# Kernel tuning notes

Measured on AMD Instinct MI355X. Metric: run time of the kernel, lower is better.

## Reference

```python
import jax, jax.numpy as jnp
import numpy as np

N_NODES = 20000
N_EDGES = 160000
N_GRAPHS = 64
EMB_DIM = 16
N_BASIS = 16
MAX_RADIUS = 5.0
MUL_IN = 8   # output_size: multiplicity of scalar atom features
MUL_OUT = 4  # multiplicity per output irrep (4x0e + 4x1o + 4x2e -> dim 36)
W_NUMEL = 3 * MUL_IN * MUL_IN * MUL_OUT  # 768 per-edge tensor-product weights


def setup_inputs() -> dict:
    key = jax.random.key(0)
    ks = jax.random.split(key, 16)
    pos = jax.random.normal(ks[0], (N_NODES, 3), jnp.float32) * 3.0
    A = jax.random.randint(ks[1], (N_NODES,), 0, 10)
    batch = jnp.sort(jax.random.randint(ks[2], (N_NODES,), 0, N_GRAPHS))
    edge_src = jax.random.randint(ks[3], (N_EDGES,), 0, N_NODES)
    edge_dst = jax.random.randint(ks[4], (N_EDGES,), 0, N_NODES)
    edge_shifts = jnp.zeros((N_EDGES, 3), jnp.float32)
    cell = jnp.broadcast_to(jnp.eye(3, dtype=jnp.float32) * 10.0, (N_GRAPHS, 3, 3))
    emb_table = jax.random.normal(ks[5], (10, EMB_DIM), jnp.float32)
    fit_w1 = jax.random.normal(ks[6], (EMB_DIM, 64), jnp.float32) * (2.0 / EMB_DIM) ** 0.5
    fit_b1 = jnp.zeros((64,), jnp.float32)
    fit_w2 = jax.random.normal(ks[7], (64, 32), jnp.float32) * (2.0 / 64.0) ** 0.5
    fit_b2 = jnp.zeros((32,), jnp.float32)
    fit_w3 = jax.random.normal(ks[8], (32, MUL_IN), jnp.float32) * (2.0 / 32.0) ** 0.5
    fit_b3 = jnp.zeros((MUL_IN,), jnp.float32)
    fc_w1 = jax.random.normal(ks[9], (N_BASIS, 64), jnp.float32)
    fc_w2 = jax.random.normal(ks[10], (64, 64), jnp.float32)
    fc_w3 = jax.random.normal(ks[11], (64, 64), jnp.float32)
    fc_w4 = jax.random.normal(ks[12], (64, W_NUMEL), jnp.float32)
    return dict(pos=pos, A=A, batch=batch, edge_src=edge_src, edge_dst=edge_dst,
                edge_shifts=edge_shifts, cell=cell, emb_table=emb_table,
                fit_w1=fit_w1, fit_b1=fit_b1, fit_w2=fit_w2, fit_b2=fit_b2,
                fit_w3=fit_w3, fit_b3=fit_b3,
                fc_w1=fc_w1, fc_w2=fc_w2, fc_w3=fc_w3, fc_w4=fc_w4)


def _forward(pos, edge_shifts, cell, emb_table, fit_w1, fit_b1, fit_w2, fit_b2,
             fit_w3, fit_b3, fc_w1, fc_w2, fc_w3, fc_w4, A, batch, edge_src, edge_dst):
    E = edge_src.shape[0]
    # edge vectors with periodic shifts
    shift = jnp.einsum('ni,nij->nj', edge_shifts, cell[batch[edge_src]])
    ev = pos[edge_dst] - pos[edge_src] + shift                     # [E,3]
    r = jnp.sqrt(jnp.sum(ev * ev, axis=1))                         # [E]
    v = ev / jnp.maximum(r, 1e-9)[:, None]
    x, y, z = v[:, 0], v[:, 1], v[:, 2]
    # spherical harmonics lmax=2, normalize=True, 'component' normalization (e3nn order)
    sh0 = jnp.ones_like(x)                                         # [E]
    sh1 = jnp.sqrt(3.0) * jnp.stack([y, z, x], axis=-1)            # [E,3]
    s15 = jnp.sqrt(15.0); s5 = jnp.sqrt(5.0)
    sh2 = jnp.stack([s15 * x * y, s15 * y * z, (s5 / 2.0) * (3.0 * z * z - 1.0),
                     s15 * x * z, (s15 / 2.0) * (x * x - y * y)], axis=-1)  # [E,5]
    # node scalar features: embedding + fitnet MLP (SiLU)
    h = jax.nn.silu(emb_table[A] @ fit_w1 + fit_b1)
    h = jax.nn.silu(h @ fit_w2 + fit_b2)
    Ai = h @ fit_w3 + fit_b3                                       # [N, MUL_IN]
    # soft_one_hot_linspace(gaussian, cutoff=True) * sqrt(n_basis)
    centers = jnp.linspace(0.0, MAX_RADIUS, N_BASIS + 2)[1:-1]
    step = centers[1] - centers[0]
    rb = jnp.exp(-(((r[:, None] - centers) / step) ** 2)) / 1.12 * jnp.sqrt(jnp.float32(N_BASIS))
    # radial net -> per-edge tensor-product weights (e3nn FullyConnectedNet style, no bias)
    g = jax.nn.silu(rb @ fc_w1 / jnp.sqrt(jnp.float32(N_BASIS)))
    g = jax.nn.silu(g @ fc_w2 / 8.0)
    g = jax.nn.silu(g @ fc_w3 / 8.0)
    w = (g @ fc_w4 / 8.0).reshape(E, 3, MUL_IN, MUL_IN, MUL_OUT)   # [E,3 paths,u,v,w]
    # FullTensorProduct(Ai_src, sh) then FullyConnectedTensorProduct(., Ai_dst) with
    # per-edge weights; scalar x irrep paths factorize: out_l[e,w,m] = S_l[e,w]*sh_l[e,m]
    P = Ai[edge_src][:, :, None] * Ai[edge_dst][:, None, :]        # [E,u,v]
    S = jnp.einsum('euv,eluvw->elw', P, w) / jnp.float32(MUL_IN)   # path norm 1/sqrt(u*v)
    out0 = S[:, 0, :] * sh0[:, None]                               # [E,4]
    out1 = (S[:, 1, :, None] * sh1[:, None, :]).reshape(E, MUL_OUT * 3)
    out2 = (S[:, 2, :, None] * sh2[:, None, :]).reshape(E, MUL_OUT * 5)
    ef = jnp.concatenate([out0, out1, out2], axis=-1)              # [E,36]
    # scatter-mean to destination nodes
    cnt = jnp.clip(jax.ops.segment_sum(jnp.ones((E,), ef.dtype), edge_dst,
                                       num_segments=N_NODES), 1.0)
    return jax.ops.segment_sum(ef, edge_dst, num_segments=N_NODES) / cnt[:, None]


def reference(pos, A, batch, edge_src, edge_dst, edge_shifts, cell, emb_table,
              fit_w1, fit_b1, fit_w2, fit_b2, fit_w3, fit_b3,
              fc_w1, fc_w2, fc_w3, fc_w4):
    return _forward(pos, edge_shifts, cell, emb_table, fit_w1, fit_b1, fit_w2,
                    fit_b2, fit_w3, fit_b3, fc_w1, fc_w2, fc_w3, fc_w4,
                    A, batch, edge_src, edge_dst)
```

## Files before the change

kernel.cpp:

```cpp
#include <hip/hip_runtime.h>
#include <math.h>

#define N_NODES 20000
#define N_EDGES 160000

#define NBINS   512
#define BINS1   513
#define RMAX    7.5f

static const size_t OFF_EF  = 0;
static const size_t OFF_T   = OFF_EF  + (size_t)N_EDGES * 16 * 4;
static const size_t OFF_G   = OFF_T   + (size_t)100 * 64 * 12 * 4;
static const size_t OFF_SV  = OFF_G   + (size_t)64 * BINS1 * 4;
static const size_t OFF_NOFF= OFF_SV  + (size_t)100 * BINS1 * 12 * 4;
static const size_t OFF_NCNT= OFF_NOFF+ (size_t)(N_NODES + 1) * 4;
static const size_t OFF_NCUR= OFF_NCNT+ (size_t)N_NODES * 4;

#define P1_T_BLOCKS  25
#define P1_G_BLOCKS  9
#define P1_H_BLOCKS  625
#define P1_GRID (P1_T_BLOCKS + P1_G_BLOCKS + P1_H_BLOCKS)
#define P2_SCAN_BLOCKS 79
#define P2_CHUNKS 9
#define P2_GRID (P2_SCAN_BLOCKS + 100 * P2_CHUNKS)

__device__ __forceinline__ float silu_f(float x) {
    return x / (1.0f + __expf(-x));
}

__global__ __launch_bounds__(256) void prep1_kernel(
        const float* __restrict__ emb,
        const float* __restrict__ fw1, const float* __restrict__ fb1,
        const float* __restrict__ fw2, const float* __restrict__ fb2,
        const float* __restrict__ fw3, const float* __restrict__ fb3,
        const float* __restrict__ fc_w1, const float* __restrict__ fc_w2,
        const float* __restrict__ fc_w3, const float* __restrict__ fc_w4,
        const int* __restrict__ edst,
        float* __restrict__ T, float* __restrict__ g_tT,
        int* __restrict__ cnt_i) {
    __shared__ float smem[4096];
    int b = blockIdx.x;
    int tid = threadIdx.x;

    if (b < P1_T_BLOCKS) {
        float* h1s = smem;
        float* h2s = smem + 640;
        float* ai  = smem + 960;
        for (int idx = tid; idx < 640; idx += 256) {
            int t = idx >> 6, j = idx & 63;
            float acc = fb1[j];
            #pragma unroll
            for (int i = 0; i < 16; i++) acc += emb[t * 16 + i] * fw1[i * 64 + j];
            h1s[idx] = silu_f(acc);
        }
        __syncthreads();
        for (int idx = tid; idx < 320; idx += 256) {
            int t = idx >> 5, j = idx & 31;
            float acc = fb2[j];
            #pragma unroll
            for (int i = 0; i < 64; i++) acc += h1s[t * 64 + i] * fw2[i * 32 + j];
            h2s[idx] = silu_f(acc);
        }
        __syncthreads();
        if (tid < 80) {
            int t = tid >> 3, j = tid & 7;
            float acc = fb3[j];
            #pragma unroll
            for (int i = 0; i < 32; i++) acc += h2s[t * 32 + i] * fw3[i * 8 + j];
            ai[tid] = acc;
        }
        __syncthreads();

        int idx = b * 256 + tid;
        int pair = idx >> 6;
        int k = idx & 63;
        int ts = pair / 10, td = pair - ts * 10;
        float a[8], bb[8];
        #pragma unroll
        for (int i = 0; i < 8; i++) a[i] = ai[ts * 8 + i];
        #pragma unroll
        for (int i = 0; i < 8; i++) bb[i] = ai[td * 8 + i];
        float sv[12];
        #pragma unroll
        for (int i = 0; i < 12; i++) sv[i] = 0.0f;
        const float* wk = fc_w4 + k * 768;
        #pragma unroll 2
        for (int u = 0; u < 8; u++) {
            #pragma unroll
            for (int v = 0; v < 8; v++) {
                float ab = a[u] * bb[v];
                const float* wp = wk + u * 32 + v * 4;
                float4 w0 = *(const float4*)(wp);
                float4 w1 = *(const float4*)(wp + 256);
                float4 w2 = *(const float4*)(wp + 512);
                sv[0] += ab * w0.x; sv[1] += ab * w0.y; sv[2]  += ab * w0.z; sv[3]  += ab * w0.w;
                sv[4] += ab * w1.x; sv[5] += ab * w1.y; sv[6]  += ab * w1.z; sv[7]  += ab * w1.w;
                sv[8] += ab * w2.x; sv[9] += ab * w2.y; sv[10] += ab * w2.z; sv[11] += ab * w2.w;
            }
        }
        float* tp = T + pair * 768 + k * 12;
        #pragma unroll
        for (int j = 0; j < 12; j++) tp[j] = sv[j];
    } else if (b < P1_T_BLOCKS + P1_G_BLOCKS) {
        int lane = tid & 63;
        int wq = __builtin_amdgcn_readfirstlane(tid >> 6);
        int bin = (b - P1_T_BLOCKS) * 64 + lane;
        bool valid = (bin <= NBINS);
        float r = (float)bin * (RMAX / (float)NBINS);

        float rb[16];
        const float step = 5.0f / 17.0f;
        const float istep = 17.0f / 5.0f;
        const float rsc = 4.0f / 1.12f;
        #pragma unroll
        for (int i = 0; i < 16; i++) {
            float dd = (r - (float)(i + 1) * step) * istep;
            rb[i] = __expf(-dd * dd) * rsc;
        }

        #pragma unroll
        for (int jj = 0; jj < 16; jj++) {
            int j = wq * 16 + jj;
            float a0 = 0, a1 = 0, a2 = 0, a3 = 0;
            #pragma unroll
            for (int i = 0; i < 16; i += 4) {
                a0 += rb[i]     * fc_w1[(i)     * 64 + j];
                a1 += rb[i + 1] * fc_w1[(i + 1) * 64 + j];
                a2 += rb[i + 2] * fc_w1[(i + 2) * 64 + j];
                a3 += rb[i + 3] * fc_w1[(i + 3) * 64 + j];
            }
            smem[j * 64 + lane] = silu_f(((a0 + a1) + (a2 + a3)) * 0.25f);
        }
        __syncthreads();

        float acc[16];
        #pragma unroll
        for (int jj = 0; jj < 16; jj++) acc[jj] = 0.0f;
        #pragma unroll
        for (int c = 0; c < 4; c++) {
            float hc[16];
            #pragma unroll
            for (int i = 0; i < 16; i++) hc[i] = smem[(c * 16 + i) * 64 + lane];
            #pragma unroll
            for (int jj = 0; jj < 16; jj++) {
                int j = wq * 16 + jj;
                #pragma unroll
                for (int i = 0; i < 16; i++) acc[jj] += hc[i] * fc_w2[(c * 16 + i) * 64 + j];
            }
        }
        __syncthreads();
        #pragma unroll
        for (int jj = 0; jj < 16; jj++) smem[(wq * 16 + jj) * 64 + lane] = silu_f(acc[jj] * 0.125f);
        __syncthreads();

        #pragma unroll
        for (int jj = 0; jj < 16; jj++) acc[jj] = 0.0f;
        #pragma unroll
        for (int c = 0; c < 4; c++) {
            float hc[16];
            #pragma unroll
            for (int i = 0; i < 16; i++) hc[i] = smem[(c * 16 + i) * 64 + lane];
            #pragma unroll
            for (int jj = 0; jj < 16; jj++) {
                int j = wq * 16 + jj;
                #pragma unroll
                for (int i = 0; i < 16; i++) acc[jj] += hc[i] * fc_w3[(c * 16 + i) * 64 + j];
            }
        }
        if (valid) {
            #pragma unroll
            for (int jj = 0; jj < 16; jj++)
                g_tT[(size_t)(wq * 16 + jj) * BINS1 + bin] = silu_f(acc[jj] * 0.125f);
        }
    } else {
        int e = (b - P1_T_BLOCKS - P1_G_BLOCKS) * 256 + tid;
        if (e < N_EDGES) atomicAdd(&cnt_i[edst[e]], 1);
    }
}

__global__ __launch_bounds__(256) void prep2_kernel(
        const int* __restrict__ cnt_i, int* __restrict__ node_off,
        const float* __restrict__ T, const float* __restrict__ g_tT,
        float* __restrict__ sv_table) {
    __shared__ float smem[4096];
    int b = blockIdx.x;
    int tid = threadIdx.x;

    if (b < P2_SCAN_BLOCKS) {
        int* wred = (int*)smem;
        int* wsum = (int*)smem + 4;
        int lane = tid & 63, w = tid >> 6;
        int nbase = b * 256;
        int n = nbase + tid;
        int c = (n < N_NODES) ? cnt_i[n] : 0;

        int part = 0;
        for (int i = tid; i < nbase; i += 256) part += cnt_i[i];
        #pragma unroll
        for (int off = 1; off < 64; off <<= 1) part += __shfl_xor(part, off);
        if (lane == 0) wred[w] = part;

        int sc = c;
        #pragma unroll
        for (int off = 1; off < 64; off <<= 1) {
            int v2 = __shfl_up(sc, off);
            if (lane >= off) sc += v2;
        }
        if (lane == 63) wsum[w] = sc;
        __syncthreads();

        int base = wred[0] + wred[1] + wred[2] + wred[3];
        int wb = 0;
        #pragma unroll
        for (int i = 0; i < 4; i++) wb += (i < w) ? wsum[i] : 0;
        if (n < N_NODES) node_off[n] = base + wb + (sc - c);
        if (b == 0 && tid == 0) node_off[N_NODES] = N_EDGES;
        return;
    }

    int idx = b - P2_SCAN_BLOCKS;
    int pair = idx / P2_CHUNKS;
    int chunk = idx - pair * P2_CHUNKS;

    float* part = smem;
    float* Tlds = smem + 3328;

    const float* Tp = T + pair * 768;
    #pragma unroll
    for (int i = tid; i < 768; i += 256) Tlds[i] = Tp[i];
    __syncthreads();

    int lane = tid & 63;
    int wq = tid >> 6;
    int bin = chunk * 64 + lane;
    bool valid = (bin <= NBINS);
    int rb = valid ? bin : NBINS;

    float acc[12];
    #pragma unroll
    for (int j = 0; j < 12; j++) acc[j] = 0.0f;
    #pragma unroll
    for (int kk = 0; kk < 16; kk++) {
        int k = wq * 16 + kk;
        float g = g_tT[(size_t)k * BINS1 + rb];
        const float* Tl = Tlds + k * 12;
        #pragma unroll
        for (int j = 0; j < 12; j++) acc[j] += g * Tl[j];
    }

    float* pp = part + (size_t)wq * 64 * 13 + (size_t)lane * 13;
    #pragma unroll
    for (int j = 0; j < 12; j++) pp[j] = acc[j];
    __syncthreads();

    const float isc = 1.0f / 64.0f;
    float* svp = sv_table + (size_t)pair * BINS1 * 12 + (size_t)chunk * 64 * 12;
    #pragma unroll
    for (int i = 0; i < 3; i++) {
        int o = tid + 256 * i;
        int bl = o / 12;
        int j = o - bl * 12;
        if (chunk * 64 + bl <= NBINS) {
            float s = part[(size_t)0 * 832 + bl * 13 + j]
                    + part[(size_t)1 * 832 + bl * 13 + j]
                    + part[(size_t)2 * 832 + bl * 13 + j]
                    + part[(size_t)3 * 832 + bl * 13 + j];
            svp[o] = s * isc;
        }
    }
}

__global__ __launch_bounds__(256) void edge_table_kernel(
        const float* __restrict__ pos, const int* __restrict__ batch,
        const int* __restrict__ esrc, const int* __restrict__ edst,
        const float* __restrict__ shifts, const float* __restrict__ cell,
        const int* __restrict__ A,
        const int* __restrict__ node_off, int* __restrict__ node_cur,
        const float* __restrict__ sv_table, float* __restrict__ ef) {
    int e = blockIdx.x * 256 + threadIdx.x;
    if (e >= N_EDGES) return;

    int s = esrc[e], d = edst[e];
    int slot = atomicAdd(&node_cur[d], 1);
    int base = node_off[d];

    int gb = batch[s];
    float t0 = shifts[e * 3 + 0], t1 = shifts[e * 3 + 1], t2 = shifts[e * 3 + 2];
    const float* C = cell + gb * 9;
    float shx = t0 * C[0] + t1 * C[3] + t2 * C[6];
    float shy = t0 * C[1] + t1 * C[4] + t2 * C[7];
    float shz = t0 * C[2] + t1 * C[5] + t2 * C[8];
    float ex = pos[d * 3 + 0] - pos[s * 3 + 0] + shx;
    float ey = pos[d * 3 + 1] - pos[s * 3 + 1] + shy;
    float ez = pos[d * 3 + 2] - pos[s * 3 + 2] + shz;
    float r = sqrtf(ex * ex + ey * ey + ez * ez);
    float inv = 1.0f / fmaxf(r, 1e-9f);
    float x = ex * inv, y = ey * inv, z = ez * inv;

    float sv[12];
    if (r >= RMAX) {
        #pragma unroll
        for (int j = 0; j < 12; j++) sv[j] = 0.0f;
    } else {
        int pair = A[s] * 10 + A[d];
        float t = r * ((float)NBINS / RMAX);
        int i = (int)t;
        i = (i > NBINS - 1) ? (NBINS - 1) : i;
        float f = t - (float)i;
        const float* r0 = sv_table + ((size_t)pair * BINS1 + i) * 12;
        #pragma unroll
        for (int j = 0; j < 12; j++) {
            float lo = r0[j], hi = r0[12 + j];
            sv[j] = lo + f * (hi - lo);
        }
    }

    float4* dst = (float4*)(ef + (size_t)(base + slot) * 16);
    dst[0] = make_float4(sv[0], sv[1], sv[2],  sv[3]);
    dst[1] = make_float4(sv[4], sv[5], sv[6],  sv[7]);
    dst[2] = make_float4(sv[8], sv[9], sv[10], sv[11]);
    dst[3] = make_float4(x, y, z, 0.0f);
}

__global__ __launch_bounds__(256) void gather_kernel(const float* __restrict__ ef,
                                                     const int* __restrict__ node_off,
                                                     float* __restrict__ out) {
    int t = blockIdx.x * 256 + threadIdx.x;
    if (t >= N_NODES * 8) return;
    int n = t >> 3;
    int q = t & 7;
    int beg = node_off[n], end = node_off[n + 1];
    const float4* ef4 = (const float4*)ef;

    const float S3  = 1.7320508075688772f;
    const float S15 = 3.8729833462074170f;
    const float S5  = 2.2360679774997896f;

    float acc[36];
    #pragma unroll
    for (int j = 0; j < 36; j++) acc[j] = 0.0f;

    for (int p = beg + q; p < end; p += 8) {
        const float4* rp = ef4 + (size_t)p * 4;
        float4 svA = rp[0];
        float4 svB = rp[1];
        float4 svC = rp[2];
        float4 dv  = rp[3];
        float x = dv.x, y = dv.y, z = dv.z;
        float sh1v[3] = { S3 * y, S3 * z, S3 * x };
        float sh2v[5] = { S15 * x * y, S15 * y * z, 0.5f * S5 * (3.0f * z * z - 1.0f),
                          S15 * x * z, 0.5f * S15 * (x * x - y * y) };
        acc[0] += svA.x; acc[1] += svA.y; acc[2] += svA.z; acc[3] += svA.w;
        float bw[4] = { svB.x, svB.y, svB.z, svB.w };
        #pragma unroll
        for (int w = 0; w < 4; w++) {
            #pragma unroll
            for (int j = 0; j < 3; j++) acc[4 + w * 3 + j] += bw[w] * sh1v[j];
        }
        float cw[4] = { svC.x, svC.y, svC.z, svC.w };
        #pragma unroll
        for (int w = 0; w < 4; w++) {
            #pragma unroll
            for (int j = 0; j < 5; j++) acc[16 + w * 5 + j] += cw[w] * sh2v[j];
        }
    }

    #pragma unroll
    for (int j = 0; j < 36; j++) {
        acc[j] += __shfl_xor(acc[j], 1);
        acc[j] += __shfl_xor(acc[j], 2);
        acc[j] += __shfl_xor(acc[j], 4);
    }

    if (q == 0) {
        float c = 1.0f / fmaxf((float)(end - beg), 1.0f);
        float4* o4 = (float4*)out + (size_t)n * 9;
        #pragma unroll
        for (int k = 0; k < 9; k++)
            o4[k] = make_float4(acc[k * 4 + 0] * c, acc[k * 4 + 1] * c,
                                acc[k * 4 + 2] * c, acc[k * 4 + 3] * c);
    }
}

extern "C" void kernel_launch(void* const* d_in, const int* in_sizes, int n_in,
                              void* d_out, int out_size, void* d_ws, size_t ws_size,
                              hipStream_t stream) {
    const float* pos    = (const float*)d_in[0];
    const int*   A      = (const int*)d_in[1];
    const int*   batch  = (const int*)d_in[2];
    const int*   esrc   = (const int*)d_in[3];
    const int*   edst   = (const int*)d_in[4];
    const float* shifts = (const float*)d_in[5];
    const float* cell   = (const float*)d_in[6];
    const float* emb    = (const float*)d_in[7];
    const float* fw1    = (const float*)d_in[8];
    const float* fb1    = (const float*)d_in[9];
    const float* fw2    = (const float*)d_in[10];
    const float* fb2    = (const float*)d_in[11];
    const float* fw3    = (const float*)d_in[12];
    const float* fb3    = (const float*)d_in[13];
    const float* fcw1   = (const float*)d_in[14];
    const float* fcw2   = (const float*)d_in[15];
    const float* fcw3   = (const float*)d_in[16];
    const float* fcw4   = (const float*)d_in[17];
    float* out = (float*)d_out;

    char* ws = (char*)d_ws;
    float* ef      = (float*)(ws + OFF_EF);
    float* T       = (float*)(ws + OFF_T);
    float* g_tT    = (float*)(ws + OFF_G);
    float* sv_table= (float*)(ws + OFF_SV);
    int*   node_off= (int*)(ws + OFF_NOFF);
    int*   cnt_i   = (int*)(ws + OFF_NCNT);
    int*   node_cur= (int*)(ws + OFF_NCUR);

    hipMemsetAsync(cnt_i, 0, (size_t)2 * N_NODES * 4, stream);

    prep1_kernel<<<P1_GRID, 256, 0, stream>>>(emb, fw1, fb1, fw2, fb2, fw3, fb3,
                                              fcw1, fcw2, fcw3, fcw4, edst,
                                              T, g_tT, cnt_i);
    prep2_kernel<<<P2_GRID, 256, 0, stream>>>(cnt_i, node_off, T, g_tT, sv_table);
    edge_table_kernel<<<(N_EDGES + 255) / 256, 256, 0, stream>>>(
        pos, batch, esrc, edst, shifts, cell, A, node_off, node_cur, sv_table, ef);
    gather_kernel<<<(N_NODES * 8 + 255) / 256, 256, 0, stream>>>(ef, node_off, out);
}
```

Baseline: 163.7 us.

## Fuse four pipeline kernels into one cooperative persistent kernel with grid syncs

Merges the prep1, prep2, edge-table and gather kernels into a single cooperative kernel of 640 persistent blocks. Each block loops over the old virtual block indices and the phases are separated by grid.sync() instead of kernel boundaries. This targets launch overhead and inter-kernel gaps. In exchange it adds grid-wide barrier cost, reduces parallelism in phases that previously had more blocks, and adds extra __syncthreads for shared-memory reuse. The old four-launch path remains as a fallback if the cooperative launch fails.

```diff
diff --git a/kernel.cpp b/kernel.cpp
--- a/kernel.cpp
+++ b/kernel.cpp
@@ -1,5 +1,8 @@
 #include <hip/hip_runtime.h>
+#include <hip/hip_cooperative_groups.h>
 #include <math.h>
+
+namespace cg = cooperative_groups;
 
 #define N_NODES 20000
 #define N_EDGES 160000
@@ -24,11 +27,14 @@
 #define P2_CHUNKS 9
 #define P2_GRID (P2_SCAN_BLOCKS + 100 * P2_CHUNKS)
 
+#define FGRID 640
+
 __device__ __forceinline__ float silu_f(float x) {
     return x / (1.0f + __expf(-x));
 }
 
-__global__ __launch_bounds__(256) void prep1_kernel(
+
+__device__ __forceinline__ void phaseA_body(int bb, int tid, float* smem,
         const float* __restrict__ emb,
         const float* __restrict__ fw1, const float* __restrict__ fb1,
         const float* __restrict__ fw2, const float* __restrict__ fb2,
@@ -38,11 +44,7 @@
         const int* __restrict__ edst,
         float* __restrict__ T, float* __restrict__ g_tT,
         int* __restrict__ cnt_i) {
-    __shared__ float smem[4096];
-    int b = blockIdx.x;
-    int tid = threadIdx.x;
-
-    if (b < P1_T_BLOCKS) {
+    if (bb < P1_T_BLOCKS) {
         float* h1s = smem;
         float* h2s = smem + 640;
         float* ai  = smem + 960;
@@ -71,15 +73,15 @@
         }
         __syncthreads();
 
-        int idx = b * 256 + tid;
+        int idx = bb * 256 + tid;
         int pair = idx >> 6;
         int k = idx & 63;
         int ts = pair / 10, td = pair - ts * 10;
-        float a[8], bb[8];
+        float a[8], bbv[8];
         #pragma unroll
         for (int i = 0; i < 8; i++) a[i] = ai[ts * 8 + i];
         #pragma unroll
-        for (int i = 0; i < 8; i++) bb[i] = ai[td * 8 + i];
+        for (int i = 0; i < 8; i++) bbv[i] = ai[td * 8 + i];
         float sv[12];
         #pragma unroll
         for (int i = 0; i < 12; i++) sv[i] = 0.0f;
@@ -88,7 +90,7 @@
         for (int u = 0; u < 8; u++) {
             #pragma unroll
             for (int v = 0; v < 8; v++) {
-                float ab = a[u] * bb[v];
+                float ab = a[u] * bbv[v];
                 const float* wp = wk + u * 32 + v * 4;
                 float4 w0 = *(const float4*)(wp);
                 float4 w1 = *(const float4*)(wp + 256);
@@ -101,10 +103,11 @@
         float* tp = T + pair * 768 + k * 12;
         #pragma unroll
         for (int j = 0; j < 12; j++) tp[j] = sv[j];
-    } else if (b < P1_T_BLOCKS + P1_G_BLOCKS) {
+        __syncthreads();
+    } else if (bb < P1_T_BLOCKS + P1_G_BLOCKS) {
         int lane = tid & 63;
         int wq = __builtin_amdgcn_readfirstlane(tid >> 6);
-        int bin = (b - P1_T_BLOCKS) * 64 + lane;
+        int bin = (bb - P1_T_BLOCKS) * 64 + lane;
         bool valid = (bin <= NBINS);
         float r = (float)bin * (RMAX / (float)NBINS);
 
@@ -172,25 +175,22 @@
             for (int jj = 0; jj < 16; jj++)
                 g_tT[(size_t)(wq * 16 + jj) * BINS1 + bin] = silu_f(acc[jj] * 0.125f);
         }
+        __syncthreads();
     } else {
-        int e = (b - P1_T_BLOCKS - P1_G_BLOCKS) * 256 + tid;
+        int e = (bb - P1_T_BLOCKS - P1_G_BLOCKS) * 256 + tid;
         if (e < N_EDGES) atomicAdd(&cnt_i[edst[e]], 1);
     }
 }
 
-__global__ __launch_bounds__(256) void prep2_kernel(
+__device__ __forceinline__ void phaseB_body(int bb, int tid, float* smem,
         const int* __restrict__ cnt_i, int* __restrict__ node_off,
         const float* __restrict__ T, const float* __restrict__ g_tT,
         float* __restrict__ sv_table) {
-    __shared__ float smem[4096];
-    int b = blockIdx.x;
-    int tid = threadIdx.x;
-
-    if (b < P2_SCAN_BLOCKS) {
+    if (bb < P2_SCAN_BLOCKS) {
         int* wred = (int*)smem;
         int* wsum = (int*)smem + 4;
         int lane = tid & 63, w = tid >> 6;
-        int nbase = b * 256;
+        int nbase = bb * 256;
         int n = nbase + tid;
         int c = (n < N_NODES) ? cnt_i[n] : 0;
 
@@ -214,11 +214,12 @@
         #pragma unroll
         for (int i = 0; i < 4; i++) wb += (i < w) ? wsum[i] : 0;
         if (n < N_NODES) node_off[n] = base + wb + (sc - c);
-        if (b == 0 && tid == 0) node_off[N_NODES] = N_EDGES;
+        if (bb == 0 && tid == 0) node_off[N_NODES] = N_EDGES;
+        __syncthreads();
         return;
     }
 
-    int idx = b - P2_SCAN_BLOCKS;
+    int idx = bb - P2_SCAN_BLOCKS;
     int pair = idx / P2_CHUNKS;
     int chunk = idx - pair * P2_CHUNKS;
 
@@ -268,18 +269,16 @@
             svp[o] = s * isc;
         }
     }
-}
-
-__global__ __launch_bounds__(256) void edge_table_kernel(
+    __syncthreads();
+}
+
+__device__ __forceinline__ void edge_body(int e,
         const float* __restrict__ pos, const int* __restrict__ batch,
         const int* __restrict__ esrc, const int* __restrict__ edst,
         const float* __restrict__ shifts, const float* __restrict__ cell,
         const int* __restrict__ A,
         const int* __restrict__ node_off, int* __restrict__ node_cur,
         const float* __restrict__ sv_table, float* __restrict__ ef) {
-    int e = blockIdx.x * 256 + threadIdx.x;
-    if (e >= N_EDGES) return;
-
     int s = esrc[e], d = edst[e];
     int slot = atomicAdd(&node_cur[d], 1);
     int base = node_off[d];
@@ -322,11 +321,9 @@
     dst[3] = make_float4(x, y, z, 0.0f);
 }
 
-__global__ __launch_bounds__(256) void gather_kernel(const float* __restrict__ ef,
-                                                     const int* __restrict__ node_off,
-                                                     float* __restrict__ out) {
-    int t = blockIdx.x * 256 + threadIdx.x;
-    if (t >= N_NODES * 8) return;
+__device__ __forceinline__ void gather_body(int t,
+        const float* __restrict__ ef, const int* __restrict__ node_off,
+        float* __restrict__ out) {
     int n = t >> 3;
     int q = t & 7;
     int beg = node_off[n], end = node_off[n + 1];
@@ -380,6 +377,88 @@
             o4[k] = make_float4(acc[k * 4 + 0] * c, acc[k * 4 + 1] * c,
                                 acc[k * 4 + 2] * c, acc[k * 4 + 3] * c);
     }
+}
+
+__global__ __launch_bounds__(256, 4) void fused_kernel(
+        const float* __restrict__ emb,
+        const float* __restrict__ fw1, const float* __restrict__ fb1,
+        const float* __restrict__ fw2, const float* __restrict__ fb2,
+        const float* __restrict__ fw3, const float* __restrict__ fb3,
+        const float* __restrict__ fcw1, const float* __restrict__ fcw2,
+        const float* __restrict__ fcw3, const float* __restrict__ fcw4,
+        const float* __restrict__ pos, const int* __restrict__ batch,
+        const int* __restrict__ esrc, const int* __restrict__ edst,
+        const float* __restrict__ shifts, const float* __restrict__ cell,
+        const int* __restrict__ A,
+        float* __restrict__ T, float* __restrict__ g_tT,
+        float* __restrict__ sv_table, int* __restrict__ node_off,
+        int* __restrict__ cnt_i, int* __restrict__ node_cur,
+        float* __restrict__ ef, float* __restrict__ out) {
+    cg::grid_group grid = cg::this_grid();
+    __shared__ float smem[4096];
+    int b = blockIdx.x;
+    int tid = threadIdx.x;
+
+    for (int bb = b; bb < P1_GRID; bb += FGRID)
+        phaseA_body(bb, tid, smem, emb, fw1, fb1, fw2, fb2, fw3, fb3,
+                    fcw1, fcw2, fcw3, fcw4, edst, T, g_tT, cnt_i);
+    grid.sync();
+
+    for (int bb = b; bb < P2_GRID; bb += FGRID)
+        phaseB_body(bb, tid, smem, cnt_i, node_off, T, g_tT, sv_table);
+    grid.sync();
+
+    for (int e = b * 256 + tid; e < N_EDGES; e += FGRID * 256)
+        edge_body(e, pos, batch, esrc, edst, shifts, cell, A,
+                  node_off, node_cur, sv_table, ef);
+    grid.sync();
+
+    for (int t = b * 256 + tid; t < N_NODES * 8; t += FGRID * 256)
+        gather_body(t, ef, node_off, out);
+}
+
+__global__ __launch_bounds__(256) void prep1_kernel(
+        const float* __restrict__ emb,
+        const float* __restrict__ fw1, const float* __restrict__ fb1,
+        const float* __restrict__ fw2, const float* __restrict__ fb2,
+        const float* __restrict__ fw3, const float* __restrict__ fb3,
+        const float* __restrict__ fcw1, const float* __restrict__ fcw2,
+        const float* __restrict__ fcw3, const float* __restrict__ fcw4,
+        const int* __restrict__ edst,
+        float* __restrict__ T, float* __restrict__ g_tT,
+        int* __restrict__ cnt_i) {
+    __shared__ float smem[4096];
+    phaseA_body(blockIdx.x, threadIdx.x, smem, emb, fw1, fb1, fw2, fb2, fw3, fb3,
+                fcw1, fcw2, fcw3, fcw4, edst, T, g_tT, cnt_i);
+}
+
+__global__ __launch_bounds__(256) void prep2_kernel(
+        const int* __restrict__ cnt_i, int* __restrict__ node_off,
+        const float* __restrict__ T, const float* __restrict__ g_tT,
+        float* __restrict__ sv_table) {
+    __shared__ float smem[4096];
+    phaseB_body(blockIdx.x, threadIdx.x, smem, cnt_i, node_off, T, g_tT, sv_table);
+}
+
+__global__ __launch_bounds__(256) void edge_table_kernel(
+        const float* __restrict__ pos, const int* __restrict__ batch,
+        const int* __restrict__ esrc, const int* __restrict__ edst,
+        const float* __restrict__ shifts, const float* __restrict__ cell,
+        const int* __restrict__ A,
+        const int* __restrict__ node_off, int* __restrict__ node_cur,
+        const float* __restrict__ sv_table, float* __restrict__ ef) {
+    int e = blockIdx.x * 256 + threadIdx.x;
+    if (e >= N_EDGES) return;
+    edge_body(e, pos, batch, esrc, edst, shifts, cell, A,
+              node_off, node_cur, sv_table, ef);
+}
+
+__global__ __launch_bounds__(256) void gather_kernel(const float* __restrict__ ef,
+                                                     const int* __restrict__ node_off,
+                                                     float* __restrict__ out) {
+    int t = blockIdx.x * 256 + threadIdx.x;
+    if (t >= N_NODES * 8) return;
+    gather_body(t, ef, node_off, out);
 }
 
 extern "C" void kernel_launch(void* const* d_in, const int* in_sizes, int n_in,
@@ -416,11 +495,24 @@
 
     hipMemsetAsync(cnt_i, 0, (size_t)2 * N_NODES * 4, stream);
 
-    prep1_kernel<<<P1_GRID, 256, 0, stream>>>(emb, fw1, fb1, fw2, fb2, fw3, fb3,
-                                              fcw1, fcw2, fcw3, fcw4, edst,
-                                              T, g_tT, cnt_i);
-    prep2_kernel<<<P2_GRID, 256, 0, stream>>>(cnt_i, node_off, T, g_tT, sv_table);
-    edge_table_kernel<<<(N_EDGES + 255) / 256, 256, 0, stream>>>(
-        pos, batch, esrc, edst, shifts, cell, A, node_off, node_cur, sv_table, ef);
-    gather_kernel<<<(N_NODES * 8 + 255) / 256, 256, 0, stream>>>(ef, node_off, out);
-}
+    void* args[] = {
+        (void*)&emb, (void*)&fw1, (void*)&fb1, (void*)&fw2, (void*)&fb2,
+        (void*)&fw3, (void*)&fb3, (void*)&fcw1, (void*)&fcw2, (void*)&fcw3,
+        (void*)&fcw4, (void*)&pos, (void*)&batch, (void*)&esrc, (void*)&edst,
+        (void*)&shifts, (void*)&cell, (void*)&A, (void*)&T, (void*)&g_tT,
+        (void*)&sv_table, (void*)&node_off, (void*)&cnt_i, (void*)&node_cur,
+        (void*)&ef, (void*)&out
+    };
+    hipError_t err = hipLaunchCooperativeKernel((const void*)fused_kernel,
+                                                dim3(FGRID), dim3(256),
+                                                args, 0, stream);
+    if (err != hipSuccess) {
+        prep1_kernel<<<P1_GRID, 256, 0, stream>>>(emb, fw1, fb1, fw2, fb2, fw3, fb3,
+                                                  fcw1, fcw2, fcw3, fcw4, edst,
+                                                  T, g_tT, cnt_i);
+        prep2_kernel<<<P2_GRID, 256, 0, stream>>>(cnt_i, node_off, T, g_tT, sv_table);
+        edge_table_kernel<<<(N_EDGES + 255) / 256, 256, 0, stream>>>(
+            pos, batch, esrc, edst, shifts, cell, A, node_off, node_cur, sv_table, ef);
+        gather_kernel<<<(N_NODES * 8 + 255) / 256, 256, 0, stream>>>(ef, node_off, out);
+    }
+}
```

Result: slower. 459.5 us (+180.7%).
